# Kernel optimization log

Hardware: AMD Instinct MI355X
Metric: run time of the kernel (lower is better)

Reference implementation:

```python
import jax, jax.numpy as jnp
import numpy as np
from jax import lax

V, E, H, MLP, NCLS = 50000, 100, 100, 300, 3
B, T, C = 256, 128, 255


def _lstm_dir(x, Wih, Whh, bih, bhh, reverse):
    # x: [T, B, E]; PyTorch gate order i, f, g, o
    Bsz = x.shape[1]
    h0 = jnp.zeros((Bsz, H), x.dtype)
    c0 = jnp.zeros((Bsz, H), x.dtype)

    def step(carry, xt):
        h, c = carry
        gates = xt @ Wih.T + h @ Whh.T + (bih + bhh)  # [B, 4H]
        i, f, g, o = jnp.split(gates, 4, axis=-1)
        c = jax.nn.sigmoid(f) * c + jax.nn.sigmoid(i) * jnp.tanh(g)
        h = jax.nn.sigmoid(o) * jnp.tanh(c)
        return (h, c), h

    _, hs = lax.scan(step, (h0, c0), x, reverse=reverse)
    return hs  # [T, B, H]


def setup_inputs() -> dict:
    key = jax.random.key(0)
    ks = jax.random.split(key, 16)
    s_e = 1.0 / np.sqrt(H)
    inp = {
        "x": jax.random.randint(ks[0], (B, T), 0, V),
        "paths": jax.random.randint(ks[1], (B, C, 3), 0, T),
        "emb": jax.random.normal(ks[2], (V, E), jnp.float32),
        "Wih_f": jax.random.uniform(ks[3], (4 * H, E), jnp.float32, -s_e, s_e),
        "Whh_f": jax.random.uniform(ks[4], (4 * H, H), jnp.float32, -s_e, s_e),
        "bih_f": jax.random.uniform(ks[5], (4 * H,), jnp.float32, -s_e, s_e),
        "bhh_f": jax.random.uniform(ks[6], (4 * H,), jnp.float32, -s_e, s_e),
        "Wih_b": jax.random.uniform(ks[7], (4 * H, E), jnp.float32, -s_e, s_e),
        "Whh_b": jax.random.uniform(ks[8], (4 * H, H), jnp.float32, -s_e, s_e),
        "bih_b": jax.random.uniform(ks[9], (4 * H,), jnp.float32, -s_e, s_e),
        "bhh_b": jax.random.uniform(ks[10], (4 * H,), jnp.float32, -s_e, s_e),
        "W1": jax.random.normal(ks[11], (6 * H, MLP), jnp.float32) * 0.05,
        "b1": jnp.zeros((MLP,), jnp.float32),
        "W2": jax.random.normal(ks[12], (MLP, NCLS), jnp.float32) * 0.05,
        "b2": jnp.zeros((NCLS,), jnp.float32),
    }
    return inp


def reference(x, paths, emb, Wih_f, Whh_f, bih_f, bhh_f, Wih_b, Whh_b, bih_b, bhh_b, W1, b1, W2, b2):
    # embedding lookup (dropout is eval-mode identity)
    xe = emb[x]                      # [B, T, E]
    xe = jnp.transpose(xe, (1, 0, 2))  # [T, B, E] (seq-major like packed LSTM)
    hf = _lstm_dir(xe, Wih_f, Whh_f, bih_f, bhh_f, reverse=False)
    hb = _lstm_dir(xe, Wih_b, Whh_b, bih_b, bhh_b, reverse=True)
    h = jnp.concatenate([hf, hb], axis=-1)        # [T, B, 2H]
    hbt = jnp.transpose(h, (1, 0, 2))             # [B, T, 2H]
    # gather 3 positions per configuration; index -1 -> zero vector
    idx = jnp.clip(paths, 0, T - 1)               # [B, C, 3]
    g = hbt[jnp.arange(hbt.shape[0])[:, None, None], idx]  # [B, C, 3, 2H]
    g = jnp.where((paths >= 0)[..., None], g, 0.0)
    mlp_in = g.reshape(-1, 6 * H)                 # [B*C, 600]
    hdn = jnp.tanh(mlp_in @ W1 + b1)
    return jax.nn.softmax(hdn @ W2 + b2, axis=-1)  # [B*C, 3]
```

## Files before the change

### kernel.cpp

```cpp
#include <hip/hip_runtime.h>

typedef unsigned short u16;
typedef short short8 __attribute__((ext_vector_type(8)));
typedef float f32x4 __attribute__((ext_vector_type(4)));

__device__ __forceinline__ u16 f2b(float x){
  union{float f; unsigned u;} v; v.f = x;
  unsigned r = (v.u + 0x7FFFu + ((v.u >> 16) & 1u)) >> 16;
  return (u16)r;
}
__device__ __forceinline__ float b2f(u16 h){
  union{unsigned u; float f;} v; v.u = ((unsigned)h) << 16; return v.f;
}
__device__ __forceinline__ float sigm(float x){ return 1.0f/(1.0f + __expf(-x)); }
__device__ __forceinline__ float tanh_f(float x){ return 1.0f - 2.0f/(1.0f + __expf(2.0f*x)); }

__global__ void prep_kernel(const int* __restrict__ x, const float* __restrict__ emb,
   const float* __restrict__ Wih_f, const float* __restrict__ Whh_f,
   const float* __restrict__ bih_f, const float* __restrict__ bhh_f,
   const float* __restrict__ Wih_b, const float* __restrict__ Whh_b,
   const float* __restrict__ bih_b, const float* __restrict__ bhh_b,
   const float* __restrict__ W1,
   u16* __restrict__ xe, u16* __restrict__ wc, float* __restrict__ biasC,
   float* __restrict__ whhT, u16* __restrict__ w1b, u16* __restrict__ hbt)
{
  int id = blockIdx.x*256 + threadIdx.x;
  const int N0 = 32768*128;
  const int N1 = 832*128;
  const int N2 = 800;
  const int N3 = 80000;
  const int N4 = 672*320;
  const int N5 = 32768*24;
  if (id < N0){
    int p = id >> 7, k = id & 127;
    float v = 0.f;
    if (k < 100) v = emb[x[p]*100 + k];
    xe[id] = f2b(v);
    return;
  }
  id -= N0;
  if (id < N1){
    int n = id >> 7, k = id & 127;
    float v = 0.f;
    if (k < 100){
      if (n < 400) v = Wih_f[n*100+k];
      else if (n < 800) v = Wih_b[(n-400)*100+k];
    }
    wc[id] = f2b(v);
    return;
  }
  id -= N1;
  if (id < N2){
    biasC[id] = (id < 400) ? (bih_f[id]+bhh_f[id]) : (bih_b[id-400]+bhh_b[id-400]);
    return;
  }
  id -= N2;
  if (id < N3){
    int d = id / 40000; int rem = id - d*40000; int k = rem / 400; int j = rem - k*400;
    const float* W = d ? Whh_b : Whh_f;
    whhT[id] = W[j*100 + k];
    return;
  }
  id -= N3;
  if (id < N4){
    int k = id / 320; int n = id - k*320;
    int seg = k / 224; int wwk = k - seg*224;
    float v = 0.f;
    if (n < 300 && wwk < 200) v = W1[(seg*200 + wwk)*300 + n];
    w1b[n*672 + k] = f2b(v);
    return;
  }
  id -= N4;
  if (id < N5){
    int p = id / 24; int k = id - p*24;
    hbt[p*224 + 200 + k] = 0;
  }
}

__global__ __launch_bounds__(256) void gemm1_kernel(const u16* __restrict__ xe,
    const u16* __restrict__ wc, const float* __restrict__ biasC, u16* __restrict__ inp)
{
  __shared__ __align__(16) u16 As[64*136];
  __shared__ __align__(16) u16 Bs[64*136];
  const int m0 = blockIdx.x*64, n0 = blockIdx.y*64;
  const int tid = threadIdx.x;
  #pragma unroll
  for (int i=0;i<4;i++){
    int f = i*256 + tid;
    int row = f >> 4, c8 = f & 15;
    *(uint4*)&As[row*136 + c8*8] = *(const uint4*)&xe[(m0+row)*128 + c8*8];
    *(uint4*)&Bs[row*136 + c8*8] = *(const uint4*)&wc[(n0+row)*128 + c8*8];
  }
  __syncthreads();
  const int w = tid >> 6, lane = tid & 63, col = lane & 15, quad = lane >> 4;
  f32x4 acc[4];
  #pragma unroll
  for (int nt=0;nt<4;nt++) acc[nt] = (f32x4){0.f,0.f,0.f,0.f};
  #pragma unroll
  for (int kc=0;kc<4;kc++){
    short8 af = *(const short8*)&As[(w*16+col)*136 + kc*32 + quad*8];
    #pragma unroll
    for (int nt=0;nt<4;nt++){
      short8 bfrag = *(const short8*)&Bs[(nt*16+col)*136 + kc*32 + quad*8];
      acc[nt] = __builtin_amdgcn_mfma_f32_16x16x32_bf16(af, bfrag, acc[nt], 0, 0, 0);
    }
  }
  #pragma unroll
  for (int nt=0;nt<4;nt++){
    int n = n0 + nt*16 + col;
    if (n < 800){
      float bs = biasC[n];
      int dir = (n >= 400) ? 1 : 0;
      int j = n - dir*400;
      #pragma unroll
      for (int r=0;r<4;r++){
        int m = m0 + w*16 + quad*4 + r;
        inp[(dir*32768 + m)*400 + j] = f2b(acc[nt][r] + bs);
      }
    }
  }
}

__global__ __launch_bounds__(448, 2) void lstm_kernel(const u16* __restrict__ inp,
    const float* __restrict__ whhT, u16* __restrict__ hbt)
{
  const int cid = blockIdx.x;
  const int b = cid & 255, dir = cid >> 8;
  const int jj = threadIdx.x;
  __shared__ __align__(16) float hs[104];
  __shared__ float act[400];
  float whh[100];
  if (jj < 400){
    const float* wp = whhT + dir*40000 + jj;
    #pragma unroll
    for (int k=0;k<100;k++) whh[k] = wp[k*400];
  }
  if (jj < 104) hs[jj] = 0.f;
  float c = 0.f;
  const u16* ipt = inp + (dir*32768 + b*128)*400 + (dir ? 127*400 : 0);
  u16* hpt = hbt + b*128*224 + (dir ? 127*224 : 0) + dir*100 + jj;
  const int dIp = dir ? -400 : 400;
  const int dHp = dir ? -224 : 224;
  u16 curraw = (jj < 400) ? ipt[jj] : (u16)0;
  __syncthreads();
  for (int step=0; step<128; step++){
    if (jj < 400){
      float pre = b2f(curraw);
      if (step < 127) curraw = ipt[dIp + jj];
      ipt += dIp;
      const float4* h4 = (const float4*)hs;
      float a0=0.f,a1=0.f,a2=0.f,a3=0.f;
      #pragma unroll
      for (int kk=0;kk<25;kk++){
        float4 hv = h4[kk];
        a0 = fmaf(whh[4*kk+0], hv.x, a0);
        a1 = fmaf(whh[4*kk+1], hv.y, a1);
        a2 = fmaf(whh[4*kk+2], hv.z, a2);
        a3 = fmaf(whh[4*kk+3], hv.w, a3);
      }
      float xg = pre + ((a0+a1)+(a2+a3));
      act[jj] = (jj >= 200 && jj < 300) ? tanh_f(xg) : sigm(xg);
    }
    __syncthreads();
    if (jj < 100){
      float ig = act[jj], fg = act[100+jj], gg = act[200+jj], og = act[300+jj];
      c = fg*c + ig*gg;
      float hk = og * tanh_f(c);
      hs[jj] = hk;
      *hpt = f2b(hk);
      hpt += dHp;
    }
    __syncthreads();
  }
}

__global__ __launch_bounds__(512) void mlp_kernel(const u16* __restrict__ hbt,
    const u16* __restrict__ w1b, const int* __restrict__ paths,
    const float* __restrict__ b1, const float* __restrict__ W2,
    const float* __restrict__ b2, float* __restrict__ out)
{
  __shared__ __align__(16) u16 As[128*40];
  __shared__ __align__(16) u16 Bs[320*40];
  const int m0 = blockIdx.x*128;
  const int tid = threadIdx.x;
  const int arow = tid >> 2, ac8 = tid & 3;
  const int am = m0 + arow;
  const int ab = am / 255;
  const int w = tid >> 6, lane = tid & 63, col = lane & 15, quad = lane >> 4;
  f32x4 acc[20];
  #pragma unroll
  for (int nt=0;nt<20;nt++) acc[nt] = (f32x4){0.f,0.f,0.f,0.f};
  for (int kc=0;kc<21;kc++){
    __syncthreads();
    for (int f = tid; f < 1280; f += 512){
      int br = f >> 2, bc = f & 3;
      *(uint4*)&Bs[br*40 + bc*8] = *(const uint4*)&w1b[br*672 + kc*32 + bc*8];
    }
    int seg = (kc >= 14) ? 2 : (kc >= 7 ? 1 : 0);
    int ko = kc - seg*7;
    int it = paths[am*3 + seg];
    uint4 v = make_uint4(0u,0u,0u,0u);
    if (it >= 0){
      int t = it > 127 ? 127 : it;
      v = *(const uint4*)&hbt[(ab*128 + t)*224 + ko*32 + ac8*8];
    }
    *(uint4*)&As[arow*40 + ac8*8] = v;
    __syncthreads();
    short8 af = *(const short8*)&As[(w*16+col)*40 + quad*8];
    #pragma unroll
    for (int nt=0;nt<20;nt++){
      short8 bfrag = *(const short8*)&Bs[(nt*16+col)*40 + quad*8];
      acc[nt] = __builtin_amdgcn_mfma_f32_16x16x32_bf16(af, bfrag, acc[nt], 0, 0, 0);
    }
  }
  float pz[4][3];
  #pragma unroll
  for (int r=0;r<4;r++){ pz[r][0]=0.f; pz[r][1]=0.f; pz[r][2]=0.f; }
  #pragma unroll
  for (int nt=0;nt<20;nt++){
    int n = nt*16 + col;
    if (n < 300){
      float bb = b1[n];
      float w20 = W2[n*3+0], w21 = W2[n*3+1], w22 = W2[n*3+2];
      #pragma unroll
      for (int r=0;r<4;r++){
        float hdn = tanh_f(acc[nt][r] + bb);
        pz[r][0] = fmaf(hdn, w20, pz[r][0]);
        pz[r][1] = fmaf(hdn, w21, pz[r][1]);
        pz[r][2] = fmaf(hdn, w22, pz[r][2]);
      }
    }
  }
  #pragma unroll
  for (int off=1; off<16; off<<=1){
    #pragma unroll
    for (int r=0;r<4;r++){
      pz[r][0] += __shfl_xor(pz[r][0], off, 64);
      pz[r][1] += __shfl_xor(pz[r][1], off, 64);
      pz[r][2] += __shfl_xor(pz[r][2], off, 64);
    }
  }
  float c0 = b2[0], c1 = b2[1], c2 = b2[2];
  #pragma unroll
  for (int r=0;r<4;r++){
    float z0 = pz[r][0]+c0, z1 = pz[r][1]+c1, z2 = pz[r][2]+c2;
    float mx = fmaxf(z0, fmaxf(z1, z2));
    float e0 = __expf(z0-mx), e1 = __expf(z1-mx), e2 = __expf(z2-mx);
    float inv = 1.0f/(e0+e1+e2);
    if (col < 3){
      float pv = (col==0 ? e0 : (col==1 ? e1 : e2)) * inv;
      out[(m0 + w*16 + quad*4 + r)*3 + col] = pv;
    }
  }
}

extern "C" void kernel_launch(void* const* d_in, const int* in_sizes, int n_in,
                              void* d_out, int out_size, void* d_ws, size_t ws_size,
                              hipStream_t stream)
{
  const int*   x     = (const int*)  d_in[0];
  const int*   paths = (const int*)  d_in[1];
  const float* emb   = (const float*)d_in[2];
  const float* Wih_f = (const float*)d_in[3];
  const float* Whh_f = (const float*)d_in[4];
  const float* bih_f = (const float*)d_in[5];
  const float* bhh_f = (const float*)d_in[6];
  const float* Wih_b = (const float*)d_in[7];
  const float* Whh_b = (const float*)d_in[8];
  const float* bih_b = (const float*)d_in[9];
  const float* bhh_b = (const float*)d_in[10];
  const float* W1    = (const float*)d_in[11];
  const float* b1    = (const float*)d_in[12];
  const float* W2    = (const float*)d_in[13];
  const float* b2    = (const float*)d_in[14];
  float* out = (float*)d_out;

  char* ws = (char*)d_ws;
  u16*   xe    = (u16*)  (ws + 0);
  u16*   wc    = (u16*)  (ws + 8388608);
  float* biasC = (float*)(ws + 8601600);
  float* whhT  = (float*)(ws + 8604800);
  u16*   w1b   = (u16*)  (ws + 8924800);
  u16*   inp   = (u16*)  (ws + 9354880);
  u16*   hbt   = (u16*)  (ws + 61783680);

  const int prep_total = 32768*128 + 832*128 + 800 + 80000 + 672*320 + 32768*24;
  prep_kernel<<<(prep_total + 255)/256, 256, 0, stream>>>(
      x, emb, Wih_f, Whh_f, bih_f, bhh_f, Wih_b, Whh_b, bih_b, bhh_b, W1,
      xe, wc, biasC, whhT, w1b, hbt);
  gemm1_kernel<<<dim3(512, 13), 256, 0, stream>>>(xe, wc, biasC, inp);
  lstm_kernel<<<512, 448, 0, stream>>>(inp, whhT, hbt);
  mlp_kernel<<<510, 512, 0, stream>>>(hbt, w1b, paths, b1, W2, b2, out);
}
```

Baseline: 348.0 us.

## Interleave LSTM gates per unit and combine via lane shuffles, one barrier per step

Reorders the recurrent weights and the precomputed input gates so the four gates of each hidden unit sit in adjacent lanes. The gates are then combined with xor shuffles instead of a shared-memory act array, and the hidden state is double-buffered, which removes one __syncthreads per timestep from the serial recurrence. The inner dot product is also forced to v_fmac via inline asm. Each lane now does redundant sigmoid/tanh work for the cell update, and the gemm1 output layout changes to match.

```diff
diff --git a/kernel.cpp b/kernel.cpp
--- a/kernel.cpp
+++ b/kernel.cpp
@@ -14,6 +14,8 @@
 }
 __device__ __forceinline__ float sigm(float x){ return 1.0f/(1.0f + __expf(-x)); }
 __device__ __forceinline__ float tanh_f(float x){ return 1.0f - 2.0f/(1.0f + __expf(2.0f*x)); }
+
+#define FMAC_V(acc, w, h) asm("v_fmac_f32 %0, %1, %2" : "+v"(acc) : "v"(w), "v"(h))
 
 __global__ void prep_kernel(const int* __restrict__ x, const float* __restrict__ emb,
    const float* __restrict__ Wih_f, const float* __restrict__ Whh_f,
@@ -22,7 +24,7 @@
    const float* __restrict__ bih_b, const float* __restrict__ bhh_b,
    const float* __restrict__ W1,
    u16* __restrict__ xe, u16* __restrict__ wc, float* __restrict__ biasC,
-   float* __restrict__ whhT, u16* __restrict__ w1b, u16* __restrict__ hbt)
+   float* __restrict__ whhQ, u16* __restrict__ w1b, u16* __restrict__ hbt)
 {
   int id = blockIdx.x*256 + threadIdx.x;
   const int N0 = 32768*128;
@@ -56,9 +58,10 @@
   }
   id -= N2;
   if (id < N3){
-    int d = id / 40000; int rem = id - d*40000; int k = rem / 400; int j = rem - k*400;
+    int d = id / 40000; int rem = id - d*40000; int k = rem / 400; int p = rem - k*400;
+    int uu = p >> 2, gg = p & 3;
     const float* W = d ? Whh_b : Whh_f;
-    whhT[id] = W[j*100 + k];
+    whhQ[id] = W[(gg*100 + uu)*100 + k];
     return;
   }
   id -= N3;
@@ -112,62 +115,74 @@
       float bs = biasC[n];
       int dir = (n >= 400) ? 1 : 0;
       int j = n - dir*400;
+      int gg = j / 100, uu = j - gg*100;
+      int pj = uu*4 + gg;
       #pragma unroll
       for (int r=0;r<4;r++){
         int m = m0 + w*16 + quad*4 + r;
-        inp[(dir*32768 + m)*400 + j] = f2b(acc[nt][r] + bs);
+        inp[(dir*32768 + m)*400 + pj] = f2b(acc[nt][r] + bs);
       }
     }
   }
 }
 
 __global__ __launch_bounds__(448, 2) void lstm_kernel(const u16* __restrict__ inp,
-    const float* __restrict__ whhT, u16* __restrict__ hbt)
-{
+    const float* __restrict__ whhQ, u16* __restrict__ hbt)
+{
+  __shared__ __align__(16) float hs2[2][104];
   const int cid = blockIdx.x;
   const int b = cid & 255, dir = cid >> 8;
-  const int jj = threadIdx.x;
-  __shared__ __align__(16) float hs[104];
-  __shared__ float act[400];
+  const int tid = threadIdx.x;
+  const int u = tid >> 2, g = tid & 3;
+  if (tid < 104) hs2[0][tid] = 0.f;
+
   float whh[100];
-  if (jj < 400){
-    const float* wp = whhT + dir*40000 + jj;
+  const u16* ipt = inp;
+  u16* hpt = hbt;
+  u16 cur = 0;
+  float c = 0.f;
+  const int t0 = dir ? 127 : 0;
+  const int dIp = dir ? -400 : 400;
+  const int dHp = dir ? -224 : 224;
+  if (tid < 400){
+    const float* wp = whhQ + dir*40000 + tid;
     #pragma unroll
     for (int k=0;k<100;k++) whh[k] = wp[k*400];
-  }
-  if (jj < 104) hs[jj] = 0.f;
-  float c = 0.f;
-  const u16* ipt = inp + (dir*32768 + b*128)*400 + (dir ? 127*400 : 0);
-  u16* hpt = hbt + b*128*224 + (dir ? 127*224 : 0) + dir*100 + jj;
-  const int dIp = dir ? -400 : 400;
-  const int dHp = dir ? -224 : 224;
-  u16 curraw = (jj < 400) ? ipt[jj] : (u16)0;
+    ipt = inp + ((size_t)(dir*32768 + b*128 + t0))*400 + tid;
+    hpt = hbt + ((size_t)(b*128 + t0))*224 + dir*100 + u;
+    cur = *ipt;
+  }
   __syncthreads();
+
+  const bool g1 = (g & 1) != 0, g2 = (g & 2) != 0;
   for (int step=0; step<128; step++){
-    if (jj < 400){
-      float pre = b2f(curraw);
-      if (step < 127) curraw = ipt[dIp + jj];
+    const int par = step & 1;
+    if (tid < 400){
+      float pre0 = b2f(cur);
+      if (step < 127) cur = ipt[dIp];
       ipt += dIp;
-      const float4* h4 = (const float4*)hs;
+      const float4* h4 = (const float4*)&hs2[par][0];
       float a0=0.f,a1=0.f,a2=0.f,a3=0.f;
       #pragma unroll
       for (int kk=0;kk<25;kk++){
         float4 hv = h4[kk];
-        a0 = fmaf(whh[4*kk+0], hv.x, a0);
-        a1 = fmaf(whh[4*kk+1], hv.y, a1);
-        a2 = fmaf(whh[4*kk+2], hv.z, a2);
-        a3 = fmaf(whh[4*kk+3], hv.w, a3);
+        FMAC_V(a0, whh[4*kk+0], hv.x);
+        FMAC_V(a1, whh[4*kk+1], hv.y);
+        FMAC_V(a2, whh[4*kk+2], hv.z);
+        FMAC_V(a3, whh[4*kk+3], hv.w);
       }
-      float xg = pre + ((a0+a1)+(a2+a3));
-      act[jj] = (jj >= 200 && jj < 300) ? tanh_f(xg) : sigm(xg);
-    }
-    __syncthreads();
-    if (jj < 100){
-      float ig = act[jj], fg = act[100+jj], gg = act[200+jj], og = act[300+jj];
-      c = fg*c + ig*gg;
-      float hk = og * tanh_f(c);
-      hs[jj] = hk;
-      *hpt = f2b(hk);
+      float pre = pre0 + ((a0+a1)+(a2+a3));
+      float s1 = __shfl_xor(pre, 1, 64);
+      float t2 = __shfl_xor(pre, 2, 64);
+      float t3 = __shfl_xor(s1, 2, 64);
+      float iv = g2 ? (g1 ? t3 : t2) : (g1 ? s1 : pre);
+      float fv = g2 ? (g1 ? t2 : t3) : (g1 ? pre : s1);
+      float gv = g2 ? (g1 ? s1 : pre) : (g1 ? t3 : t2);
+      float ov = g2 ? (g1 ? pre : s1) : (g1 ? t2 : t3);
+      c = sigm(fv)*c + sigm(iv)*tanh_f(gv);
+      float h = sigm(ov)*tanh_f(c);
+      if (g == 0)      hs2[par^1][u] = h;
+      else if (g == 1) *hpt = f2b(h);
       hpt += dHp;
     }
     __syncthreads();
@@ -279,7 +294,7 @@
   u16*   xe    = (u16*)  (ws + 0);
   u16*   wc    = (u16*)  (ws + 8388608);
   float* biasC = (float*)(ws + 8601600);
-  float* whhT  = (float*)(ws + 8604800);
+  float* whhQ  = (float*)(ws + 8604800);
   u16*   w1b   = (u16*)  (ws + 8924800);
   u16*   inp   = (u16*)  (ws + 9354880);
   u16*   hbt   = (u16*)  (ws + 61783680);
@@ -287,8 +302,8 @@
   const int prep_total = 32768*128 + 832*128 + 800 + 80000 + 672*320 + 32768*24;
   prep_kernel<<<(prep_total + 255)/256, 256, 0, stream>>>(
       x, emb, Wih_f, Whh_f, bih_f, bhh_f, Wih_b, Whh_b, bih_b, bhh_b, W1,
-      xe, wc, biasC, whhT, w1b, hbt);
+      xe, wc, biasC, whhQ, w1b, hbt);
   gemm1_kernel<<<dim3(512, 13), 256, 0, stream>>>(xe, wc, biasC, inp);
-  lstm_kernel<<<512, 448, 0, stream>>>(inp, whhT, hbt);
+  lstm_kernel<<<512, 448, 0, stream>>>(inp, whhQ, hbt);
   mlp_kernel<<<510, 512, 0, stream>>>(hbt, w1b, paths, b1, W2, b2, out);
 }
```

New measurement: 500.9 us. +43.9%, slower.
